# Performance work log

Measured on AMD Instinct MI355X. Metric: run time of the kernel, lower is better.

Reference implementation:

```python
import jax, jax.numpy as jnp
import numpy as np

B, T, N, C = 4, 2048, 4, 1024   # batch, seq, expansion_rate, hidden_dim
A = 8                            # max_lora_adapters
SINKHORN_ITERS = 20
EPS = 1e-05


def _logit(x):
    x = jnp.clip(x, 1e-06, 1.0 - 1e-06)
    return jnp.log(x) - jnp.log(1.0 - x)


def setup_inputs() -> dict:
    key = jax.random.key(0)
    ks = jax.random.split(key, 12)
    nC = N * C
    x = jax.random.normal(ks[0], (B, T, N, C), dtype=jnp.float32)
    adapter_indices = jax.random.randint(ks[1], (B,), 0, A)
    # Learned parameters (perturbed from the identity init so gradients are non-trivial)
    input_norm_weight = 1.0 + 0.02 * jax.random.normal(ks[2], (A, nC), dtype=jnp.float32)
    phi_pre = 0.02 * jax.random.normal(ks[3], (A, nC, N), dtype=jnp.float32)
    phi_post = 0.02 * jax.random.normal(ks[4], (A, nC, N), dtype=jnp.float32)
    phi_res = 0.02 * jax.random.normal(ks[5], (A, nC, N * N), dtype=jnp.float32)
    b_pre = _logit(jnp.float32(1.0 / N)) + 0.1 * jax.random.normal(ks[6], (A, N), dtype=jnp.float32)
    b_post = 0.1 * jax.random.normal(ks[7], (A, N), dtype=jnp.float32)
    b_res = 10.0 * jnp.eye(N, dtype=jnp.float32) + jax.random.normal(ks[8], (A, N, N), dtype=jnp.float32)
    alpha_pre = 1.0 + 0.1 * jax.random.normal(ks[9], (A,), dtype=jnp.float32)
    alpha_post = 1.0 + 0.1 * jax.random.normal(ks[10], (A,), dtype=jnp.float32)
    alpha_res = 1.0 + 0.1 * jax.random.normal(ks[11], (A,), dtype=jnp.float32)
    return {
        "x": x,
        "input_norm_weight": input_norm_weight,
        "phi_pre": phi_pre, "phi_post": phi_post, "phi_res": phi_res,
        "b_pre": b_pre, "b_post": b_post, "b_res": b_res,
        "alpha_pre": alpha_pre, "alpha_post": alpha_post, "alpha_res": alpha_res,
        "adapter_indices": adapter_indices,
    }


def _sinkhorn_knopp(M, iters):
    M = jnp.exp(M)
    def step(_, mat):
        mat = mat / mat.sum(axis=-1, keepdims=True)
        mat = mat / mat.sum(axis=-2, keepdims=True)
        return mat
    return jax.lax.fori_loop(0, iters, step, M)


def reference(x, input_norm_weight, phi_pre, phi_post, phi_res,
              b_pre, b_post, b_res, alpha_pre, alpha_post, alpha_res,
              adapter_indices):
    Bb, Tt, n, Cc = x.shape
    idx = adapter_indices.astype(jnp.int32)
    x_flat = x.reshape(Bb, Tt, n * Cc)
    # adapter-indexed RMSNorm
    w = input_norm_weight[idx]                                  # [B, nC]
    rms = jnp.sqrt(jnp.mean(x_flat ** 2, axis=-1, keepdims=True) + EPS)
    x_norm = w[:, None, :] * x_flat / rms                       # [B, T, nC]
    # pre: input-dependent aggregation weights H_pre
    pre_logits = jnp.einsum('btd,bdn->btn', x_norm, phi_pre[idx])
    H_pre = jax.nn.sigmoid(alpha_pre[idx][:, None, None] * pre_logits + b_pre[idx][:, None, :])
    x_agg = (H_pre[..., None] * x).sum(axis=-2)                 # [B, T, C]
    output = x_agg                                              # identity block between pre and post
    # post: distribution weights H_post and doubly-stochastic mixing M
    post_logits = jnp.einsum('btd,bdn->btn', x_norm, phi_post[idx])
    H_post = 2.0 * jax.nn.sigmoid(alpha_post[idx][:, None, None] * post_logits + b_post[idx][:, None, :])
    res_logits = jnp.einsum('btd,bdm->btm', x_norm, phi_res[idx]).reshape(Bb, Tt, n, n)
    tilde_H_res = alpha_res[idx][:, None, None, None] * res_logits + b_res[idx][:, None, :, :]
    M = _sinkhorn_knopp(tilde_H_res, SINKHORN_ITERS)            # [B, T, n, n]
    y_dist = H_post[..., None] * output[..., None, :]           # [B, T, n, C]
    x_mixed = jnp.einsum('btij,btjc->btic', M, x)               # [B, T, n, C]
    return x_mixed + y_dist
```

## Files before the change

### kernel.cpp

```cpp
#include <hip/hip_runtime.h>


#define BT 8192
#define NC 4096
#define NC4 1024

__global__ __launch_bounds__(256) void lora_connector_kernel(
    const float* __restrict__ x,
    const float* __restrict__ inw,
    const float* __restrict__ phi_pre,
    const float* __restrict__ phi_post,
    const float* __restrict__ phi_res,
    const float* __restrict__ b_pre,
    const float* __restrict__ b_post,
    const float* __restrict__ b_res,
    const float* __restrict__ alpha_pre,
    const float* __restrict__ alpha_post,
    const float* __restrict__ alpha_res,
    const int*   __restrict__ adapter_indices,
    float* __restrict__ out)
{
    const int tid = threadIdx.x;
    const int g   = tid & 3;
    const int l   = tid >> 2;
    const int tok = blockIdx.x * 4 + g;
    const int b   = blockIdx.x >> 9;
    const int idx = adapter_indices[b];

    const float4* __restrict__ x4p = (const float4*)x + (size_t)tok * NC4;
    const float4* __restrict__ w4p = (const float4*)inw + (size_t)idx * NC4;
    const float4* __restrict__ pp4 = (const float4*)(phi_pre  + (size_t)idx * (NC * 4));
    const float4* __restrict__ po4 = (const float4*)(phi_post + (size_t)idx * (NC * 4));
    const float4* __restrict__ pr4 = (const float4*)(phi_res  + (size_t)idx * (NC * 16));

    float4 xs[16];
    float acc[25];
    #pragma unroll
    for (int j = 0; j < 25; ++j) acc[j] = 0.0f;

    #pragma unroll
    for (int m = 0; m < 16; ++m) {
        const int d4 = m * 64 + l;
        const float4 xv = x4p[d4];
        const float4 wv = w4p[d4];
        xs[m] = xv;
        acc[24] = fmaf(xv.x, xv.x, fmaf(xv.y, xv.y, fmaf(xv.z, xv.z, fmaf(xv.w, xv.w, acc[24]))));
        const float xw[4] = { xv.x * wv.x, xv.y * wv.y, xv.z * wv.z, xv.w * wv.w };
        #pragma unroll
        for (int e = 0; e < 4; ++e) {
            const int d = d4 * 4 + e;
            const float s = xw[e];
            const float4 a = pp4[d];
            acc[0] = fmaf(s, a.x, acc[0]);
            acc[1] = fmaf(s, a.y, acc[1]);
            acc[2] = fmaf(s, a.z, acc[2]);
            acc[3] = fmaf(s, a.w, acc[3]);
            const float4 p = po4[d];
            acc[4] = fmaf(s, p.x, acc[4]);
            acc[5] = fmaf(s, p.y, acc[5]);
            acc[6] = fmaf(s, p.z, acc[6]);
            acc[7] = fmaf(s, p.w, acc[7]);
            #pragma unroll
            for (int q = 0; q < 4; ++q) {
                const float4 r = pr4[d * 4 + q];
                acc[8 + q * 4 + 0] = fmaf(s, r.x, acc[8 + q * 4 + 0]);
                acc[8 + q * 4 + 1] = fmaf(s, r.y, acc[8 + q * 4 + 1]);
                acc[8 + q * 4 + 2] = fmaf(s, r.z, acc[8 + q * 4 + 2]);
                acc[8 + q * 4 + 3] = fmaf(s, r.w, acc[8 + q * 4 + 3]);
            }
        }
    }

    #pragma unroll
    for (int j = 0; j < 25; ++j) {
        float v = acc[j];
        v += __shfl_xor(v, 4);
        v += __shfl_xor(v, 8);
        v += __shfl_xor(v, 16);
        v += __shfl_xor(v, 32);
        acc[j] = v;
    }

    __shared__ float red[4][4][26];
    const int wv = tid >> 6;
    const int lw = tid & 63;
    if ((lw >> 2) == 0) {
        #pragma unroll
        for (int j = 0; j < 25; ++j) red[wv][g][j] = acc[j];
    }
    __syncthreads();
    float tot[25];
    #pragma unroll
    for (int j = 0; j < 25; ++j)
        tot[j] = (red[0][g][j] + red[1][g][j]) + (red[2][g][j] + red[3][g][j]);

    const float inv_rms = rsqrtf(tot[24] * (1.0f / 4096.0f) + 1e-5f);
    const float apre  = alpha_pre[idx];
    const float apost = alpha_post[idx];
    const float ares  = alpha_res[idx];

    float Hpre[4], Hpost[4];
    #pragma unroll
    for (int n = 0; n < 4; ++n) {
        const float zp = fmaf(apre,  tot[n]     * inv_rms, b_pre[idx * 4 + n]);
        Hpre[n]  = 1.0f / (1.0f + __expf(-zp));
        const float zq = fmaf(apost, tot[4 + n] * inv_rms, b_post[idx * 4 + n]);
        Hpost[n] = 2.0f / (1.0f + __expf(-zq));
    }

    const int s  = lw >> 2;
    const int sj = s & 3;
    const int si = s >> 2;
    float Mv = __expf(fmaf(ares, tot[8 + si * 4 + sj] * inv_rms,
                           b_res[idx * 16 + si * 4 + sj]));
    #pragma unroll
    for (int it = 0; it < 20; ++it) {
        float rs = Mv + __shfl_xor(Mv, 4);
        rs += __shfl_xor(rs, 8);
        Mv *= __builtin_amdgcn_rcpf(rs);
        float cs = Mv + __shfl_xor(Mv, 16);
        cs += __shfl_xor(cs, 32);
        Mv *= __builtin_amdgcn_rcpf(cs);
    }

    float W[4][4];
    #pragma unroll
    for (int ss = 0; ss < 16; ++ss) {
        const float mm = __shfl(Mv, ss * 4 + g);
        W[ss >> 2][ss & 3] = fmaf(Hpost[ss >> 2], Hpre[ss & 3], mm);
    }

    float4* __restrict__ out4 = (float4*)out + (size_t)tok * NC4;
    #pragma unroll
    for (int k = 0; k < 4; ++k) {
        const int c4 = k * 64 + l;
        const float4 x0 = xs[0 * 4 + k];
        const float4 x1 = xs[1 * 4 + k];
        const float4 x2 = xs[2 * 4 + k];
        const float4 x3 = xs[3 * 4 + k];
        #pragma unroll
        for (int i = 0; i < 4; ++i) {
            float4 o;
            o.x = fmaf(W[i][0], x0.x, fmaf(W[i][1], x1.x, fmaf(W[i][2], x2.x, W[i][3] * x3.x)));
            o.y = fmaf(W[i][0], x0.y, fmaf(W[i][1], x1.y, fmaf(W[i][2], x2.y, W[i][3] * x3.y)));
            o.z = fmaf(W[i][0], x0.z, fmaf(W[i][1], x1.z, fmaf(W[i][2], x2.z, W[i][3] * x3.z)));
            o.w = fmaf(W[i][0], x0.w, fmaf(W[i][1], x1.w, fmaf(W[i][2], x2.w, W[i][3] * x3.w)));
            out4[i * 256 + c4] = o;
        }
    }
}

extern "C" void kernel_launch(void* const* d_in, const int* in_sizes, int n_in,
                              void* d_out, int out_size, void* d_ws, size_t ws_size,
                              hipStream_t stream) {
    const float* x         = (const float*)d_in[0];
    const float* inw       = (const float*)d_in[1];
    const float* phi_pre   = (const float*)d_in[2];
    const float* phi_post  = (const float*)d_in[3];
    const float* phi_res   = (const float*)d_in[4];
    const float* b_pre     = (const float*)d_in[5];
    const float* b_post    = (const float*)d_in[6];
    const float* b_res     = (const float*)d_in[7];
    const float* alpha_pre = (const float*)d_in[8];
    const float* alpha_post= (const float*)d_in[9];
    const float* alpha_res = (const float*)d_in[10];
    const int*   adapter   = (const int*)d_in[11];
    float* out = (float*)d_out;

    dim3 grid(BT / 4);
    dim3 block(256);
    lora_connector_kernel<<<grid, block, 0, stream>>>(
        x, inw, phi_pre, phi_post, phi_res,
        b_pre, b_post, b_res,
        alpha_pre, alpha_post, alpha_res,
        adapter, out);
}
```

Measured before the change: 360.2 us.

## Process 16 tokens per block to amortize phi weight loads, reload x for output

```diff
diff --git a/kernel.cpp b/kernel.cpp
--- a/kernel.cpp
+++ b/kernel.cpp
@@ -1,11 +1,10 @@
 #include <hip/hip_runtime.h>
 
 
-#define BT 8192
-#define NC 4096
 #define NC4 1024
+#define GTOK 16
 
-__global__ __launch_bounds__(256) void lora_connector_kernel(
+__global__ __launch_bounds__(512, 4) void lora_connector_kernel(
     const float* __restrict__ x,
     const float* __restrict__ inw,
     const float* __restrict__ phi_pre,
@@ -21,29 +20,26 @@
     float* __restrict__ out)
 {
     const int tid = threadIdx.x;
-    const int g   = tid & 3;
-    const int l   = tid >> 2;
-    const int tok = blockIdx.x * 4 + g;
-    const int b   = blockIdx.x >> 9;
-    const int idx = adapter_indices[b];
+    const int g   = tid & 15;
+    const int l   = tid >> 4;
+    const int tok = blockIdx.x * GTOK + g;
+    const int idx = adapter_indices[blockIdx.x >> 7];
 
     const float4* __restrict__ x4p = (const float4*)x + (size_t)tok * NC4;
     const float4* __restrict__ w4p = (const float4*)inw + (size_t)idx * NC4;
-    const float4* __restrict__ pp4 = (const float4*)(phi_pre  + (size_t)idx * (NC * 4));
-    const float4* __restrict__ po4 = (const float4*)(phi_post + (size_t)idx * (NC * 4));
-    const float4* __restrict__ pr4 = (const float4*)(phi_res  + (size_t)idx * (NC * 16));
+    const float4* __restrict__ pp4 = (const float4*)phi_pre  + (size_t)idx * 4096;
+    const float4* __restrict__ po4 = (const float4*)phi_post + (size_t)idx * 4096;
+    const float4* __restrict__ pr4 = (const float4*)phi_res  + (size_t)idx * 16384;
 
-    float4 xs[16];
     float acc[25];
     #pragma unroll
     for (int j = 0; j < 25; ++j) acc[j] = 0.0f;
 
-    #pragma unroll
-    for (int m = 0; m < 16; ++m) {
-        const int d4 = m * 64 + l;
+    #pragma unroll 4
+    for (int m = 0; m < 32; ++m) {
+        const int d4 = m * 32 + l;
         const float4 xv = x4p[d4];
         const float4 wv = w4p[d4];
-        xs[m] = xv;
         acc[24] = fmaf(xv.x, xv.x, fmaf(xv.y, xv.y, fmaf(xv.z, xv.z, fmaf(xv.w, xv.w, acc[24]))));
         const float xw[4] = { xv.x * wv.x, xv.y * wv.y, xv.z * wv.z, xv.w * wv.w };
         #pragma unroll
@@ -74,70 +70,66 @@
     #pragma unroll
     for (int j = 0; j < 25; ++j) {
         float v = acc[j];
-        v += __shfl_xor(v, 4);
-        v += __shfl_xor(v, 8);
         v += __shfl_xor(v, 16);
         v += __shfl_xor(v, 32);
         acc[j] = v;
     }
 
-    __shared__ float red[4][4][26];
+    __shared__ float red[8][16][26];
+    __shared__ float Wl[16][17];
     const int wv = tid >> 6;
     const int lw = tid & 63;
-    if ((lw >> 2) == 0) {
+    if (lw < 16) {
         #pragma unroll
-        for (int j = 0; j < 25; ++j) red[wv][g][j] = acc[j];
+        for (int j = 0; j < 25; ++j) red[wv][lw][j] = acc[j];
     }
     __syncthreads();
-    float tot[25];
-    #pragma unroll
-    for (int j = 0; j < 25; ++j)
-        tot[j] = (red[0][g][j] + red[1][g][j]) + (red[2][g][j] + red[3][g][j]);
 
-    const float inv_rms = rsqrtf(tot[24] * (1.0f / 4096.0f) + 1e-5f);
-    const float apre  = alpha_pre[idx];
-    const float apost = alpha_post[idx];
-    const float ares  = alpha_res[idx];
+    if (tid < 256) {
+        const int tau = tid >> 4;
+        const int sig = tid & 15;
+        const int si  = sig >> 2;
+        const int sj  = sig & 3;
+        float t_res = 0.f, t_ss = 0.f, t_pre = 0.f, t_post = 0.f;
+        #pragma unroll
+        for (int w = 0; w < 8; ++w) {
+            t_res  += red[w][tau][8 + sig];
+            t_ss   += red[w][tau][24];
+            t_pre  += red[w][tau][sj];
+            t_post += red[w][tau][4 + si];
+        }
+        const float inv_rms = rsqrtf(t_ss * (1.0f / 4096.0f) + 1e-5f);
+        const float zp = fmaf(alpha_pre[idx],  t_pre  * inv_rms, b_pre[idx * 4 + sj]);
+        const float Hpre = 1.0f / (1.0f + __expf(-zp));
+        const float zq = fmaf(alpha_post[idx], t_post * inv_rms, b_post[idx * 4 + si]);
+        const float Hpost = 2.0f / (1.0f + __expf(-zq));
 
-    float Hpre[4], Hpost[4];
-    #pragma unroll
-    for (int n = 0; n < 4; ++n) {
-        const float zp = fmaf(apre,  tot[n]     * inv_rms, b_pre[idx * 4 + n]);
-        Hpre[n]  = 1.0f / (1.0f + __expf(-zp));
-        const float zq = fmaf(apost, tot[4 + n] * inv_rms, b_post[idx * 4 + n]);
-        Hpost[n] = 2.0f / (1.0f + __expf(-zq));
+        float Mv = __expf(fmaf(alpha_res[idx], t_res * inv_rms, b_res[idx * 16 + sig]));
+        #pragma unroll
+        for (int it = 0; it < 20; ++it) {
+            float rs = Mv + __shfl_xor(Mv, 1);
+            rs += __shfl_xor(rs, 2);
+            Mv *= __builtin_amdgcn_rcpf(rs);
+            float cs = Mv + __shfl_xor(Mv, 4);
+            cs += __shfl_xor(cs, 8);
+            Mv *= __builtin_amdgcn_rcpf(cs);
+        }
+        Wl[tau][sig] = fmaf(Hpost, Hpre, Mv);
     }
-
-    const int s  = lw >> 2;
-    const int sj = s & 3;
-    const int si = s >> 2;
-    float Mv = __expf(fmaf(ares, tot[8 + si * 4 + sj] * inv_rms,
-                           b_res[idx * 16 + si * 4 + sj]));
-    #pragma unroll
-    for (int it = 0; it < 20; ++it) {
-        float rs = Mv + __shfl_xor(Mv, 4);
-        rs += __shfl_xor(rs, 8);
-        Mv *= __builtin_amdgcn_rcpf(rs);
-        float cs = Mv + __shfl_xor(Mv, 16);
-        cs += __shfl_xor(cs, 32);
-        Mv *= __builtin_amdgcn_rcpf(cs);
-    }
+    __syncthreads();
 
     float W[4][4];
     #pragma unroll
-    for (int ss = 0; ss < 16; ++ss) {
-        const float mm = __shfl(Mv, ss * 4 + g);
-        W[ss >> 2][ss & 3] = fmaf(Hpost[ss >> 2], Hpre[ss & 3], mm);
-    }
+    for (int ss = 0; ss < 16; ++ss) W[ss >> 2][ss & 3] = Wl[g][ss];
 
     float4* __restrict__ out4 = (float4*)out + (size_t)tok * NC4;
-    #pragma unroll
-    for (int k = 0; k < 4; ++k) {
-        const int c4 = k * 64 + l;
-        const float4 x0 = xs[0 * 4 + k];
-        const float4 x1 = xs[1 * 4 + k];
-        const float4 x2 = xs[2 * 4 + k];
-        const float4 x3 = xs[3 * 4 + k];
+    #pragma unroll 2
+    for (int k = 0; k < 8; ++k) {
+        const int c4 = k * 32 + l;
+        const float4 x0 = x4p[c4];
+        const float4 x1 = x4p[256 + c4];
+        const float4 x2 = x4p[512 + c4];
+        const float4 x3 = x4p[768 + c4];
         #pragma unroll
         for (int i = 0; i < 4; ++i) {
             float4 o;
@@ -167,8 +159,8 @@
     const int*   adapter   = (const int*)d_in[11];
     float* out = (float*)d_out;
 
-    dim3 grid(BT / 4);
-    dim3 block(256);
+    dim3 grid(8192 / GTOK);
+    dim3 block(512);
     lora_connector_kernel<<<grid, block, 0, stream>>>(
         x, inw, phi_pre, phi_post, phi_res,
         b_pre, b_post, b_res,
```

After: 415.1 us. 1.15x slower.

## Stage phi weights in shared memory and map one token per wavefront

Applied to the files above, without the earlier changes.

```diff
diff --git a/kernel.cpp b/kernel.cpp
--- a/kernel.cpp
+++ b/kernel.cpp
@@ -1,11 +1,9 @@
 #include <hip/hip_runtime.h>
 
 
-#define BT 8192
-#define NC 4096
 #define NC4 1024
 
-__global__ __launch_bounds__(256) void lora_connector_kernel(
+__global__ __launch_bounds__(256, 3) void lora_connector_kernel(
     const float* __restrict__ x,
     const float* __restrict__ inw,
     const float* __restrict__ phi_pre,
@@ -21,59 +19,77 @@
     float* __restrict__ out)
 {
     const int tid = threadIdx.x;
-    const int g   = tid & 3;
-    const int l   = tid >> 2;
-    const int tok = blockIdx.x * 4 + g;
-    const int b   = blockIdx.x >> 9;
-    const int idx = adapter_indices[b];
+    const int l   = tid & 63;
+    const int wv  = tid >> 6;
+    const int tok = blockIdx.x * 4 + wv;
+    const int idx = adapter_indices[blockIdx.x >> 9];
+
+    __shared__ float s_pp[4][256];
+    __shared__ float s_po[4][256];
+    __shared__ float s_pr[16][256];
 
     const float4* __restrict__ x4p = (const float4*)x + (size_t)tok * NC4;
     const float4* __restrict__ w4p = (const float4*)inw + (size_t)idx * NC4;
-    const float4* __restrict__ pp4 = (const float4*)(phi_pre  + (size_t)idx * (NC * 4));
-    const float4* __restrict__ po4 = (const float4*)(phi_post + (size_t)idx * (NC * 4));
-    const float4* __restrict__ pr4 = (const float4*)(phi_res  + (size_t)idx * (NC * 16));
+    const float4* __restrict__ pp4 = (const float4*)phi_pre  + (size_t)idx * 4096;
+    const float4* __restrict__ po4 = (const float4*)phi_post + (size_t)idx * 4096;
+    const float4* __restrict__ pr4 = (const float4*)phi_res  + (size_t)idx * 16384;
 
     float4 xs[16];
     float acc[25];
     #pragma unroll
     for (int j = 0; j < 25; ++j) acc[j] = 0.0f;
+    #pragma unroll
+    for (int m = 0; m < 16; ++m) {
+        const float4 xv = x4p[m * 64 + l];
+        xs[m] = xv;
+        acc[24] = fmaf(xv.x, xv.x, fmaf(xv.y, xv.y, fmaf(xv.z, xv.z, fmaf(xv.w, xv.w, acc[24]))));
+    }
 
     #pragma unroll
     for (int m = 0; m < 16; ++m) {
-        const int d4 = m * 64 + l;
-        const float4 xv = x4p[d4];
-        const float4 wv = w4p[d4];
-        xs[m] = xv;
-        acc[24] = fmaf(xv.x, xv.x, fmaf(xv.y, xv.y, fmaf(xv.z, xv.z, fmaf(xv.w, xv.w, acc[24]))));
-        const float xw[4] = { xv.x * wv.x, xv.y * wv.y, xv.z * wv.z, xv.w * wv.w };
+        if (m) __syncthreads();
+        {
+            const float4 a = pp4[m * 256 + tid];
+            s_pp[0][tid] = a.x; s_pp[1][tid] = a.y; s_pp[2][tid] = a.z; s_pp[3][tid] = a.w;
+            const float4 p = po4[m * 256 + tid];
+            s_po[0][tid] = p.x; s_po[1][tid] = p.y; s_po[2][tid] = p.z; s_po[3][tid] = p.w;
+            #pragma unroll
+            for (int k = 0; k < 4; ++k) {
+                const int j  = k * 256 + tid;
+                const float4 r = pr4[m * 1024 + j];
+                const int dl = j >> 2;
+                const int q  = j & 3;
+                const int col = dl ^ ((q & 1) << 4);
+                s_pr[4 * q + 0][col] = r.x;
+                s_pr[4 * q + 1][col] = r.y;
+                s_pr[4 * q + 2][col] = r.z;
+                s_pr[4 * q + 3][col] = r.w;
+            }
+        }
+        __syncthreads();
+        const float4 xv = xs[m];
+        const float4 wg = w4p[m * 64 + l];
+        const float4 xw = { xv.x * wg.x, xv.y * wg.y, xv.z * wg.z, xv.w * wg.w };
         #pragma unroll
-        for (int e = 0; e < 4; ++e) {
-            const int d = d4 * 4 + e;
-            const float s = xw[e];
-            const float4 a = pp4[d];
-            acc[0] = fmaf(s, a.x, acc[0]);
-            acc[1] = fmaf(s, a.y, acc[1]);
-            acc[2] = fmaf(s, a.z, acc[2]);
-            acc[3] = fmaf(s, a.w, acc[3]);
-            const float4 p = po4[d];
-            acc[4] = fmaf(s, p.x, acc[4]);
-            acc[5] = fmaf(s, p.y, acc[5]);
-            acc[6] = fmaf(s, p.z, acc[6]);
-            acc[7] = fmaf(s, p.w, acc[7]);
-            #pragma unroll
-            for (int q = 0; q < 4; ++q) {
-                const float4 r = pr4[d * 4 + q];
-                acc[8 + q * 4 + 0] = fmaf(s, r.x, acc[8 + q * 4 + 0]);
-                acc[8 + q * 4 + 1] = fmaf(s, r.y, acc[8 + q * 4 + 1]);
-                acc[8 + q * 4 + 2] = fmaf(s, r.z, acc[8 + q * 4 + 2]);
-                acc[8 + q * 4 + 3] = fmaf(s, r.w, acc[8 + q * 4 + 3]);
-            }
+        for (int n = 0; n < 4; ++n) {
+            const float4 a = ((const float4*)s_pp[n])[l];
+            acc[n]     = fmaf(xw.x, a.x, fmaf(xw.y, a.y, fmaf(xw.z, a.z, fmaf(xw.w, a.w, acc[n]))));
+            const float4 p = ((const float4*)s_po[n])[l];
+            acc[4 + n] = fmaf(xw.x, p.x, fmaf(xw.y, p.y, fmaf(xw.z, p.z, fmaf(xw.w, p.w, acc[4 + n]))));
+        }
+        #pragma unroll
+        for (int n = 0; n < 16; ++n) {
+            const int col4 = l ^ (((n >> 2) & 1) << 2);
+            const float4 r = ((const float4*)s_pr[n])[col4];
+            acc[8 + n] = fmaf(xw.x, r.x, fmaf(xw.y, r.y, fmaf(xw.z, r.z, fmaf(xw.w, r.w, acc[8 + n]))));
         }
     }
 
     #pragma unroll
     for (int j = 0; j < 25; ++j) {
         float v = acc[j];
+        v += __shfl_xor(v, 1);
+        v += __shfl_xor(v, 2);
         v += __shfl_xor(v, 4);
         v += __shfl_xor(v, 8);
         v += __shfl_xor(v, 16);
@@ -81,59 +97,39 @@
         acc[j] = v;
     }
 
-    __shared__ float red[4][4][26];
-    const int wv = tid >> 6;
-    const int lw = tid & 63;
-    if ((lw >> 2) == 0) {
-        #pragma unroll
-        for (int j = 0; j < 25; ++j) red[wv][g][j] = acc[j];
-    }
-    __syncthreads();
-    float tot[25];
-    #pragma unroll
-    for (int j = 0; j < 25; ++j)
-        tot[j] = (red[0][g][j] + red[1][g][j]) + (red[2][g][j] + red[3][g][j]);
-
-    const float inv_rms = rsqrtf(tot[24] * (1.0f / 4096.0f) + 1e-5f);
+    const float inv_rms = rsqrtf(acc[24] * (1.0f / 4096.0f) + 1e-5f);
     const float apre  = alpha_pre[idx];
     const float apost = alpha_post[idx];
     const float ares  = alpha_res[idx];
-
     float Hpre[4], Hpost[4];
     #pragma unroll
     for (int n = 0; n < 4; ++n) {
-        const float zp = fmaf(apre,  tot[n]     * inv_rms, b_pre[idx * 4 + n]);
+        const float zp = fmaf(apre,  acc[n]     * inv_rms, b_pre[idx * 4 + n]);
         Hpre[n]  = 1.0f / (1.0f + __expf(-zp));
-        const float zq = fmaf(apost, tot[4 + n] * inv_rms, b_post[idx * 4 + n]);
+        const float zq = fmaf(apost, acc[4 + n] * inv_rms, b_post[idx * 4 + n]);
         Hpost[n] = 2.0f / (1.0f + __expf(-zq));
     }
 
-    const int s  = lw >> 2;
-    const int sj = s & 3;
-    const int si = s >> 2;
-    float Mv = __expf(fmaf(ares, tot[8 + si * 4 + sj] * inv_rms,
-                           b_res[idx * 16 + si * 4 + sj]));
+    const int sig = l & 15;
+    float Mv = __expf(fmaf(ares, acc[8 + sig] * inv_rms, b_res[idx * 16 + sig]));
     #pragma unroll
     for (int it = 0; it < 20; ++it) {
-        float rs = Mv + __shfl_xor(Mv, 4);
-        rs += __shfl_xor(rs, 8);
+        float rs = Mv + __shfl_xor(Mv, 1);
+        rs += __shfl_xor(rs, 2);
         Mv *= __builtin_amdgcn_rcpf(rs);
-        float cs = Mv + __shfl_xor(Mv, 16);
-        cs += __shfl_xor(cs, 32);
+        float cs = Mv + __shfl_xor(Mv, 4);
+        cs += __shfl_xor(cs, 8);
         Mv *= __builtin_amdgcn_rcpf(cs);
     }
 
     float W[4][4];
     #pragma unroll
-    for (int ss = 0; ss < 16; ++ss) {
-        const float mm = __shfl(Mv, ss * 4 + g);
-        W[ss >> 2][ss & 3] = fmaf(Hpost[ss >> 2], Hpre[ss & 3], mm);
-    }
+    for (int ss = 0; ss < 16; ++ss)
+        W[ss >> 2][ss & 3] = fmaf(Hpost[ss >> 2], Hpre[ss & 3], __shfl(Mv, ss));
 
     float4* __restrict__ out4 = (float4*)out + (size_t)tok * NC4;
     #pragma unroll
     for (int k = 0; k < 4; ++k) {
-        const int c4 = k * 64 + l;
         const float4 x0 = xs[0 * 4 + k];
         const float4 x1 = xs[1 * 4 + k];
         const float4 x2 = xs[2 * 4 + k];
@@ -145,7 +141,7 @@
             o.y = fmaf(W[i][0], x0.y, fmaf(W[i][1], x1.y, fmaf(W[i][2], x2.y, W[i][3] * x3.y)));
             o.z = fmaf(W[i][0], x0.z, fmaf(W[i][1], x1.z, fmaf(W[i][2], x2.z, W[i][3] * x3.z)));
             o.w = fmaf(W[i][0], x0.w, fmaf(W[i][1], x1.w, fmaf(W[i][2], x2.w, W[i][3] * x3.w)));
-            out4[i * 256 + c4] = o;
+            out4[i * 256 + k * 64 + l] = o;
         }
     }
 }
@@ -167,7 +163,7 @@
     const int*   adapter   = (const int*)d_in[11];
     float* out = (float*)d_out;
 
-    dim3 grid(BT / 4);
+    dim3 grid(2048);
     dim3 block(256);
     lora_connector_kernel<<<grid, block, 0, stream>>>(
         x, inw, phi_pre, phi_post, phi_res,
```

Measured after the change: 412.4 us. 14.5% more time.
